# Kernel optimization log

Hardware: AMD Instinct MI355X
Metric: run time of the kernel (lower is better)

The kernel has to match this reference:

```python
import jax, jax.numpy as jnp
import numpy as np

B, G, DIN, DOUT = 4096, 16, 512, 512

def setup_inputs() -> dict:
    key = jax.random.key(0)
    kx, kw, kb = jax.random.split(key, 3)
    x = jax.random.normal(kx, (B, G, DIN), dtype=jnp.float32)
    # per-group nn.Linear weight: [G, dim_out, dim_in] (torch layout)
    W = jax.random.normal(kw, (G, DOUT, DIN), dtype=jnp.float32) * (1.0 / np.sqrt(DIN))
    b = jax.random.normal(kb, (G, DOUT), dtype=jnp.float32) * 0.01
    return {"x": x, "W": W, "b": b}

def reference(x, W, b):
    # MultiLinear: independent Linear per group g; y[..., g, :] = x[..., g, :] @ W[g].T + b[g]
    # Fused as a single batched GEMM over the group dimension.
    y = jnp.einsum('bgi,goi->bgo', x, W)  # [B, G, DOUT]
    return y + b
```

## Files before the change

### kernel.cpp

```cpp
#include <hip/hip_runtime.h>
#include <hip/hip_bf16.h>


#define BATCH 4096
#define NGRP  16
#define DIN   512
#define DOUT  512

#define BM 256
#define BN 256
#define BK 64
#define NT (DIN / BK)
#define LDKA 72

typedef __bf16 bf16x8 __attribute__((ext_vector_type(8)));
typedef float  f32x4  __attribute__((ext_vector_type(4)));
typedef const __attribute__((address_space(1))) void gas_void;
typedef __attribute__((address_space(3))) void las_void;

__global__ __launch_bounds__(256)
void wcvt_kernel(const float* __restrict__ W, __bf16* __restrict__ Wb) {
    const int i = (blockIdx.x * 256 + threadIdx.x) * 8;
    f32x4 a = *(const f32x4*)(W + i);
    f32x4 b = *(const f32x4*)(W + i + 4);
    bf16x8 v;
#pragma unroll
    for (int j = 0; j < 4; ++j) { v[j] = (__bf16)a[j]; v[j + 4] = (__bf16)b[j]; }
    *(bf16x8*)(Wb + i) = v;
}

__global__ __launch_bounds__(512, 2)
void MultiLinear_48498770706571_kernel(const float* __restrict__ X,
                                       const __bf16* __restrict__ Wb,
                                       const float* __restrict__ Bias,
                                       float* __restrict__ Y) {
    const int bid = (blockIdx.x & 7) * 64 + (blockIdx.x >> 3);
    const int g   = bid >> 5;
    const int mt  = (bid >> 1) & 15;
    const int nt  = bid & 1;
    const int bm0 = mt * BM;
    const int bn0 = nt * BN;

    __shared__ __bf16 As[2][BM][LDKA];
    __shared__ __bf16 BsF[2][BN * BK];

    const int tid  = threadIdx.x;
    const int lane = tid & 63;
    const int w    = tid >> 6;
    const int wm   = (w >> 2) * 128;
    const int wn   = (w & 3) * 64;
    const int l15  = lane & 15;
    const int kq   = (lane >> 4) * 8;

    const int srow = tid >> 2;
    const int scol = (tid & 3) * 16;
    const float* pA = X + (size_t)(bm0 + srow) * (NGRP * DIN) + g * DIN + scol;
    const size_t strideA = (size_t)128 * (NGRP * DIN);

    const int drow0 = (w << 5) + (lane >> 3);
    const int dch   = lane & 7;
    const __bf16* wbase = Wb + (size_t)g * (DOUT * DIN) + (size_t)bn0 * DIN;

    f32x4 ra[2][4];

#define ISSUE_A(k0)                                                        \
    do {                                                                   \
        const f32x4* qa0 = (const f32x4*)(pA + (k0));                      \
        const f32x4* qa1 = (const f32x4*)(pA + strideA + (k0));            \
        ra[0][0] = qa0[0]; ra[0][1] = qa0[1]; ra[0][2] = qa0[2]; ra[0][3] = qa0[3]; \
        ra[1][0] = qa1[0]; ra[1][1] = qa1[1]; ra[1][2] = qa1[2]; ra[1][3] = qa1[3]; \
    } while (0)

#define CVT_WRITE_A(buf)                                                   \
    do {                                                                   \
        _Pragma("unroll")                                                  \
        for (int p = 0; p < 2; ++p) {                                      \
            bf16x8 v0, v1;                                                 \
            _Pragma("unroll")                                              \
            for (int j = 0; j < 4; ++j) {                                  \
                v0[j] = (__bf16)ra[p][0][j]; v0[j + 4] = (__bf16)ra[p][1][j]; \
                v1[j] = (__bf16)ra[p][2][j]; v1[j + 4] = (__bf16)ra[p][3][j]; \
            }                                                              \
            *(bf16x8*)&As[buf][p * 128 + srow][scol]     = v0;             \
            *(bf16x8*)&As[buf][p * 128 + srow][scol + 8] = v1;             \
        }                                                                  \
    } while (0)

#define DMA_B(kt, buf)                                                     \
    do {                                                                   \
        const size_t k0 = (size_t)(kt) * BK;                               \
        _Pragma("unroll")                                                  \
        for (int q = 0; q < 4; ++q) {                                      \
            const int row = drow0 + (q << 3);                              \
            const __bf16* gp = wbase + (size_t)row * DIN + k0              \
                               + ((dch ^ (row & 7)) << 3);                 \
            __builtin_amdgcn_global_load_lds(                              \
                (gas_void*)gp,                                             \
                (las_void*)&BsF[buf][(w << 11) + (q << 9)], 16, 0, 0);     \
        }                                                                  \
    } while (0)

#define COMPUTE(buf)                                                       \
    do {                                                                   \
        _Pragma("unroll")                                                  \
        for (int kk = 0; kk < 2; ++kk) {                                   \
            const int ko = kk * 32 + kq;                                   \
            bf16x8 af[8], bfr[4];                                          \
            _Pragma("unroll")                                              \
            for (int mi = 0; mi < 8; ++mi)                                 \
                af[mi] = *(const bf16x8*)&As[buf][wm + mi * 16 + l15][ko]; \
            _Pragma("unroll")                                              \
            for (int ni = 0; ni < 4; ++ni) {                               \
                const int brow = wn + ni * 16 + l15;                       \
                const int ch = (lane >> 4) + kk * 4;                       \
                bfr[ni] = *(const bf16x8*)&BsF[buf][brow * 64              \
                            + ((ch ^ (brow & 7)) << 3)];                   \
            }                                                              \
            _Pragma("unroll")                                              \
            for (int mi = 0; mi < 8; ++mi)                                 \
                _Pragma("unroll")                                          \
                for (int ni = 0; ni < 4; ++ni)                             \
                    acc[mi][ni] = __builtin_amdgcn_mfma_f32_16x16x32_bf16( \
                        af[mi], bfr[ni], acc[mi][ni], 0, 0, 0);            \
        }                                                                  \
    } while (0)

    f32x4 acc[8][4];
#pragma unroll
    for (int mi = 0; mi < 8; ++mi)
#pragma unroll
        for (int ni = 0; ni < 4; ++ni) acc[mi][ni] = f32x4{0.f, 0.f, 0.f, 0.f};

    ISSUE_A(0);
    DMA_B(0, 0);
    CVT_WRITE_A(0);
    ISSUE_A(BK);

    for (int kt = 0; kt < NT; ++kt) {
        const int cur = kt & 1;
        if (kt + 1 < NT)
            asm volatile("s_waitcnt vmcnt(8)" ::: "memory");
        else
            asm volatile("s_waitcnt vmcnt(0)" ::: "memory");
        asm volatile("s_waitcnt lgkmcnt(0)" ::: "memory");
        __builtin_amdgcn_s_barrier();

        if (kt + 1 < NT) DMA_B(kt + 1, cur ^ 1);

        COMPUTE(cur);

        if (kt + 1 < NT) {
            CVT_WRITE_A(cur ^ 1);
            if (kt + 2 < NT) ISSUE_A((kt + 2) * BK);
        }
    }

    const int r0 = (lane >> 4) * 4;
    const int c  = lane & 15;
    float bias_n[4];
#pragma unroll
    for (int ni = 0; ni < 4; ++ni)
        bias_n[ni] = Bias[g * DOUT + bn0 + wn + ni * 16 + c];
#pragma unroll
    for (int mi = 0; mi < 8; ++mi) {
#pragma unroll
        for (int j = 0; j < 4; ++j) {
            const int row = bm0 + wm + mi * 16 + r0 + j;
            float* yrow = Y + (size_t)row * (NGRP * DOUT) + g * DOUT + bn0 + wn;
#pragma unroll
            for (int ni = 0; ni < 4; ++ni)
                yrow[ni * 16 + c] = acc[mi][ni][j] + bias_n[ni];
        }
    }
#undef ISSUE_A
#undef CVT_WRITE_A
#undef DMA_B
#undef COMPUTE
}

extern "C" void kernel_launch(void* const* d_in, const int* in_sizes, int n_in,
                              void* d_out, int out_size, void* d_ws, size_t ws_size,
                              hipStream_t stream) {
    const float* X    = (const float*)d_in[0];
    const float* W    = (const float*)d_in[1];
    const float* Bias = (const float*)d_in[2];
    float* Y          = (float*)d_out;
    __bf16* Wb        = (__bf16*)d_ws;

    wcvt_kernel<<<2048, 256, 0, stream>>>(W, Wb);

    const int grid = NGRP * (BATCH / BM) * (DOUT / BN);
    MultiLinear_48498770706571_kernel<<<grid, 512, 0, stream>>>(X, Wb, Bias, Y);
}
```

Measured before the change: 84.04 us.

## Shrink GEMM tile to 128x256x32 and raise occupancy to four blocks per CU

Halves the M tile and K step, so each block runs a smaller 4x4 MFMA accumulator set per wave and twice as many blocks are launched. Launch bounds now target four resident blocks per CU to improve latency hiding. The B-tile LDS swizzle is redone as a rotation for the 32-wide K layout, and the A staging and wait counts are resized to match. The cost is less operand reuse per block, twice the K-loop iterations and barriers, and more global traffic for weights and activations.

```diff
diff --git a/kernel.cpp b/kernel.cpp
--- a/kernel.cpp
+++ b/kernel.cpp
@@ -7,11 +7,11 @@
 #define DIN   512
 #define DOUT  512
 
-#define BM 256
+#define BM 128
 #define BN 256
-#define BK 64
+#define BK 32
 #define NT (DIN / BK)
-#define LDKA 72
+#define LDKA 40
 
 typedef __bf16 bf16x8 __attribute__((ext_vector_type(8)));
 typedef float  f32x4  __attribute__((ext_vector_type(4)));
@@ -29,14 +29,14 @@
     *(bf16x8*)(Wb + i) = v;
 }
 
-__global__ __launch_bounds__(512, 2)
+__global__ __launch_bounds__(512, 4)
 void MultiLinear_48498770706571_kernel(const float* __restrict__ X,
                                        const __bf16* __restrict__ Wb,
                                        const float* __restrict__ Bias,
                                        float* __restrict__ Y) {
-    const int bid = (blockIdx.x & 7) * 64 + (blockIdx.x >> 3);
-    const int g   = bid >> 5;
-    const int mt  = (bid >> 1) & 15;
+    const int bid = (blockIdx.x & 7) * 128 + (blockIdx.x >> 3);
+    const int g   = bid >> 6;
+    const int mt  = (bid >> 1) & 31;
     const int nt  = bid & 1;
     const int bm0 = mt * BM;
     const int bn0 = nt * BN;
@@ -47,87 +47,74 @@
     const int tid  = threadIdx.x;
     const int lane = tid & 63;
     const int w    = tid >> 6;
-    const int wm   = (w >> 2) * 128;
+    const int wm   = (w >> 2) * 64;
     const int wn   = (w & 3) * 64;
     const int l15  = lane & 15;
     const int kq   = (lane >> 4) * 8;
 
     const int srow = tid >> 2;
-    const int scol = (tid & 3) * 16;
+    const int scol = (tid & 3) * 8;
     const float* pA = X + (size_t)(bm0 + srow) * (NGRP * DIN) + g * DIN + scol;
-    const size_t strideA = (size_t)128 * (NGRP * DIN);
 
-    const int drow0 = (w << 5) + (lane >> 3);
-    const int dch   = lane & 7;
     const __bf16* wbase = Wb + (size_t)g * (DOUT * DIN) + (size_t)bn0 * DIN;
+    const int rowg0 = (w << 5) + (lane >> 2);
+    const int posd  = lane & 3;
 
-    f32x4 ra[2][4];
+    f32x4 ra[2];
 
 #define ISSUE_A(k0)                                                        \
     do {                                                                   \
-        const f32x4* qa0 = (const f32x4*)(pA + (k0));                      \
-        const f32x4* qa1 = (const f32x4*)(pA + strideA + (k0));            \
-        ra[0][0] = qa0[0]; ra[0][1] = qa0[1]; ra[0][2] = qa0[2]; ra[0][3] = qa0[3]; \
-        ra[1][0] = qa1[0]; ra[1][1] = qa1[1]; ra[1][2] = qa1[2]; ra[1][3] = qa1[3]; \
+        const f32x4* qa = (const f32x4*)(pA + (k0));                       \
+        ra[0] = qa[0]; ra[1] = qa[1];                                      \
     } while (0)
 
 #define CVT_WRITE_A(buf)                                                   \
     do {                                                                   \
+        bf16x8 v;                                                          \
         _Pragma("unroll")                                                  \
-        for (int p = 0; p < 2; ++p) {                                      \
-            bf16x8 v0, v1;                                                 \
-            _Pragma("unroll")                                              \
-            for (int j = 0; j < 4; ++j) {                                  \
-                v0[j] = (__bf16)ra[p][0][j]; v0[j + 4] = (__bf16)ra[p][1][j]; \
-                v1[j] = (__bf16)ra[p][2][j]; v1[j + 4] = (__bf16)ra[p][3][j]; \
-            }                                                              \
-            *(bf16x8*)&As[buf][p * 128 + srow][scol]     = v0;             \
-            *(bf16x8*)&As[buf][p * 128 + srow][scol + 8] = v1;             \
+        for (int j = 0; j < 4; ++j) {                                      \
+            v[j] = (__bf16)ra[0][j]; v[j + 4] = (__bf16)ra[1][j];          \
         }                                                                  \
+        *(bf16x8*)&As[buf][srow][scol] = v;                                \
     } while (0)
 
 #define DMA_B(kt, buf)                                                     \
     do {                                                                   \
-        const size_t k0 = (size_t)(kt) * BK;                               \
         _Pragma("unroll")                                                  \
-        for (int q = 0; q < 4; ++q) {                                      \
-            const int row = drow0 + (q << 3);                              \
-            const __bf16* gp = wbase + (size_t)row * DIN + k0              \
-                               + ((dch ^ (row & 7)) << 3);                 \
+        for (int q = 0; q < 2; ++q) {                                      \
+            const int rowg = rowg0 + (q << 4);                             \
+            const int csrc = (posd + 4 - ((rowg >> 1) & 3)) & 3;           \
+            const __bf16* gp = wbase + (size_t)rowg * DIN + (kt) * BK      \
+                               + (csrc << 3);                              \
             __builtin_amdgcn_global_load_lds(                              \
                 (gas_void*)gp,                                             \
-                (las_void*)&BsF[buf][(w << 11) + (q << 9)], 16, 0, 0);     \
+                (las_void*)&BsF[buf][(w << 10) + (q << 9)], 16, 0, 0);     \
         }                                                                  \
     } while (0)
 
 #define COMPUTE(buf)                                                       \
     do {                                                                   \
+        bf16x8 af[4], bfr[4];                                              \
         _Pragma("unroll")                                                  \
-        for (int kk = 0; kk < 2; ++kk) {                                   \
-            const int ko = kk * 32 + kq;                                   \
-            bf16x8 af[8], bfr[4];                                          \
+        for (int mi = 0; mi < 4; ++mi)                                     \
+            af[mi] = *(const bf16x8*)&As[buf][wm + mi * 16 + l15][kq];     \
+        _Pragma("unroll")                                                  \
+        for (int ni = 0; ni < 4; ++ni) {                                   \
+            const int brow = wn + ni * 16 + l15;                           \
+            const int pos = ((lane >> 4) + ((brow >> 1) & 3)) & 3;         \
+            bfr[ni] = *(const bf16x8*)&BsF[buf][brow * 32 + (pos << 3)];   \
+        }                                                                  \
+        _Pragma("unroll")                                                  \
+        for (int mi = 0; mi < 4; ++mi)                                     \
             _Pragma("unroll")                                              \
-            for (int mi = 0; mi < 8; ++mi)                                 \
-                af[mi] = *(const bf16x8*)&As[buf][wm + mi * 16 + l15][ko]; \
-            _Pragma("unroll")                                              \
-            for (int ni = 0; ni < 4; ++ni) {                               \
-                const int brow = wn + ni * 16 + l15;                       \
-                const int ch = (lane >> 4) + kk * 4;                       \
-                bfr[ni] = *(const bf16x8*)&BsF[buf][brow * 64              \
-                            + ((ch ^ (brow & 7)) << 3)];                   \
-            }                                                              \
-            _Pragma("unroll")                                              \
-            for (int mi = 0; mi < 8; ++mi)                                 \
-                _Pragma("unroll")                                          \
-                for (int ni = 0; ni < 4; ++ni)                             \
-                    acc[mi][ni] = __builtin_amdgcn_mfma_f32_16x16x32_bf16( \
-                        af[mi], bfr[ni], acc[mi][ni], 0, 0, 0);            \
-        }                                                                  \
+            for (int ni = 0; ni < 4; ++ni)                                 \
+                acc[mi][ni] = __builtin_amdgcn_mfma_f32_16x16x32_bf16(     \
+                    af[mi], bfr[ni], acc[mi][ni], 0, 0, 0);                \
     } while (0)
 
-    f32x4 acc[8][4];
+    f32x4 acc[4][4];
 #pragma unroll
-    for (int mi = 0; mi < 8; ++mi)
+    for (int mi = 0; mi < 4; ++mi)
 #pragma unroll
         for (int ni = 0; ni < 4; ++ni) acc[mi][ni] = f32x4{0.f, 0.f, 0.f, 0.f};
 
@@ -139,7 +126,7 @@
     for (int kt = 0; kt < NT; ++kt) {
         const int cur = kt & 1;
         if (kt + 1 < NT)
-            asm volatile("s_waitcnt vmcnt(8)" ::: "memory");
+            asm volatile("s_waitcnt vmcnt(2)" ::: "memory");
         else
             asm volatile("s_waitcnt vmcnt(0)" ::: "memory");
         asm volatile("s_waitcnt lgkmcnt(0)" ::: "memory");
@@ -162,7 +149,7 @@
     for (int ni = 0; ni < 4; ++ni)
         bias_n[ni] = Bias[g * DOUT + bn0 + wn + ni * 16 + c];
 #pragma unroll
-    for (int mi = 0; mi < 8; ++mi) {
+    for (int mi = 0; mi < 4; ++mi) {
 #pragma unroll
         for (int j = 0; j < 4; ++j) {
             const int row = bm0 + wm + mi * 16 + r0 + j;
```

Result: slower. 93.41 us (+11.1%).
